# Kernel optimization log

Hardware: AMD Instinct MI355X
Metric: run time of the kernel (lower is better)

Reference implementation:

```python
import jax, jax.numpy as jnp
import numpy as np

N, D, E, H, K = 4096, 512, 32, 128, 4  # tokens, d_model, n_experts, expert hidden, top-k


def setup_inputs() -> dict:
    key = jax.random.key(0)
    k0, k1, k2, k3 = jax.random.split(key, 4)
    x = jax.random.normal(k0, (N, D), dtype=jnp.float32)
    # router weights, init std = d**-0.5 (matches get_initializer std)
    expert_sel = jax.random.normal(k1, (E, D), dtype=jnp.float32) * (D ** -0.5)
    # per-expert MLP weights (Linear stores [out, in]; we keep [E, in, out] layout)
    w1 = jax.random.normal(k2, (E, D, H), dtype=jnp.float32) * (D ** -0.5)
    w2 = jax.random.normal(k3, (E, H, D), dtype=jnp.float32) * (H ** -0.5)
    return {"x": x, "expert_sel": expert_sel, "w1": w1, "w2": w2}


def reference(x, expert_sel, w1, w2):
    # routing: sigmoid selection, top-k experts per token
    scores = jax.nn.sigmoid(x @ expert_sel.T)          # [N, E]
    gate_vals, gate_idx = jax.lax.top_k(scores, K)     # [N, K]
    # dense gate matrix with only top-k nonzero (sparse dispatch/combine weights)
    gate = (jax.nn.one_hot(gate_idx, E, dtype=x.dtype) * gate_vals[..., None]).sum(-2)  # [N, E]
    # per-expert MLP; gating at hidden is exact since experts have no bias:
    # gate * (relu(x W1) W2) == (gate * relu(x W1)) W2
    h = jax.nn.relu(jnp.einsum('nd,edh->neh', x, w1)) * gate[..., None]  # [N, E, H]
    y = jnp.einsum('neh,ehv->nv', h, w2)               # [N, D]
    return y
```

## Files before the change

kernel.cpp:

```cpp
#include <hip/hip_runtime.h>
#include <hip/hip_bf16.h>

#define NTOK 4096
#define DM   512
#define NE   32
#define HD   128
#define TK   4
#define RB   512
#define SLOTW 32

typedef unsigned short u16;
typedef unsigned int   u32;
typedef u16   u16x4 __attribute__((ext_vector_type(4)));
typedef u16   u16x8 __attribute__((ext_vector_type(8)));
typedef short short8 __attribute__((ext_vector_type(8)));
typedef float f32x4 __attribute__((ext_vector_type(4)));
typedef int   int2v __attribute__((ext_vector_type(2)));

__device__ __forceinline__ u16 f2bf(float f) {
    union { float f; u32 u; } v; v.f = f;
    return (u16)((v.u + 0x7FFFu + ((v.u >> 16) & 1u)) >> 16);
}
__device__ __forceinline__ float bf2f(u16 h) {
    union { u32 u; float f; } v; v.u = ((u32)h) << 16; return v.f;
}

__global__ __launch_bounds__(256) void prep_kernel(const float* __restrict__ x,
                                                   const float* __restrict__ sel,
                                                   const float* __restrict__ w1,
                                                   const float* __restrict__ w2,
                                                   int* __restrict__ blk_cnt,
                                                   u32* __restrict__ done,
                                                   int* __restrict__ tok_list,
                                                   float* __restrict__ gate_list,
                                                   u16* __restrict__ xbf,
                                                   u16* __restrict__ wf1,
                                                   u16* __restrict__ wf2) {
    __shared__ __align__(16) float  xs[8][520];
    __shared__ double sc[8][33];
    __shared__ int    pk_e[32];
    __shared__ float  pk_g[32];
    int tid = threadIdx.x;
    int wv = tid >> 6, lane = tid & 63;

    if (blockIdx.x >= RB) {
        int m = lane & 15, q = lane >> 4;
        int f0 = ((blockIdx.x - RB) * 4 + wv) * 2;
        const float* in[2]; u16* outp[2]; int Nd[2];
#pragma unroll
        for (int u = 0; u < 2; ++u) {
            int w = f0 + u;
            if (w < 4096) {
                int e = w >> 7, rem = w & 127, ks = rem >> 3, nt = rem & 7;
                in[u] = w1 + (size_t)e * DM * HD + (size_t)(32 * ks + q * 8) * HD + 16 * nt + m;
                Nd[u] = HD;
                outp[u] = wf1 + (size_t)w * 512 + lane * 8;
            } else {
                int wl = w - 4096, e = wl >> 7, rem = wl & 127, ks = rem >> 5, nt = rem & 31;
                in[u] = w2 + (size_t)e * HD * DM + (size_t)(32 * ks + q * 8) * DM + 16 * nt + m;
                Nd[u] = DM;
                outp[u] = wf2 + (size_t)wl * 512 + lane * 8;
            }
        }
        float v[2][8];
#pragma unroll
        for (int u = 0; u < 2; ++u)
#pragma unroll
            for (int j = 0; j < 8; ++j) v[u][j] = in[u][(size_t)j * Nd[u]];
#pragma unroll
        for (int u = 0; u < 2; ++u) {
            u16x8 h;
#pragma unroll
            for (int j = 0; j < 8; ++j) h[j] = f2bf(v[u][j]);
            *(u16x8*)outp[u] = h;
        }
        return;
    }

    int bl = blockIdx.x;
    int tb = bl * 8;
    if (tid < 8) done[tb + tid] = 0u;
#pragma unroll
    for (int rep = 0; rep < 4; ++rep) {
        int idx = (rep * 256 + tid) * 4;
        int row = idx >> 9, col = idx & 511;
        f32x4 v = *(const f32x4*)(x + (size_t)(tb + row) * DM + col);
        *(f32x4*)&xs[row][col] = v;
        u16x4 h;
#pragma unroll
        for (int j = 0; j < 4; ++j) h[j] = f2bf(v[j]);
        *(u16x4*)(xbf + (size_t)(tb + row) * DM + col) = h;
    }
    __syncthreads();

    {
        int tok = tid & 7, e = tid >> 3;
        const float* sp = sel + (size_t)e * DM;
        const float* xp = xs[tok];
        double pa = 0.0, pb = 0.0, pc = 0.0, pd = 0.0;
#pragma unroll 4
        for (int j = 0; j < 512; j += 16) {
            f32x4 x0 = *(const f32x4*)(xp + j);
            f32x4 x1 = *(const f32x4*)(xp + j + 4);
            f32x4 x2 = *(const f32x4*)(xp + j + 8);
            f32x4 x3 = *(const f32x4*)(xp + j + 12);
            f32x4 s0 = *(const f32x4*)(sp + j);
            f32x4 s1 = *(const f32x4*)(sp + j + 4);
            f32x4 s2 = *(const f32x4*)(sp + j + 8);
            f32x4 s3 = *(const f32x4*)(sp + j + 12);
#pragma unroll
            for (int k = 0; k < 4; ++k) {
                pa = fma((double)x0[k], (double)s0[k], pa);
                pb = fma((double)x1[k], (double)s1[k], pb);
                pc = fma((double)x2[k], (double)s2[k], pc);
                pd = fma((double)x3[k], (double)s3[k], pd);
            }
        }
        sc[tok][e] = (pa + pb) + (pc + pd);
    }
    __syncthreads();

    if (tid < 8) {
        unsigned mask = 0;
        for (int k = 0; k < TK; ++k) {
            double best = -1e300; int be = 0;
            for (int ee = 0; ee < NE; ++ee) {
                double v = sc[tid][ee];
                if (!((mask >> ee) & 1u) && v > best) { best = v; be = ee; }
            }
            mask |= 1u << be;
            pk_e[tid * 4 + k] = be;
            pk_g[tid * 4 + k] = 1.0f / (1.0f + __expf(-(float)best));
        }
    }
    __syncthreads();

    if (tid < NE) {
        int e2 = tid, cnt = 0;
        int base = (e2 * RB + bl) * SLOTW;
#pragma unroll
        for (int i = 0; i < 32; ++i) {
            if (pk_e[i] == e2) {
                tok_list[base + cnt]  = ((i & 3) << 16) | (tb + (i >> 2));
                gate_list[base + cnt] = pk_g[i];
                ++cnt;
            }
        }
        blk_cnt[e2 * RB + bl] = cnt;
    }
}

__global__ __launch_bounds__(256, 2) void moe_mlp_kernel(const u16* __restrict__ xbf,
                                                         const u16* __restrict__ wf1,
                                                         const u16* __restrict__ wf2,
                                                         const int* __restrict__ blk_cnt,
                                                         const int* __restrict__ tok_list,
                                                         const float* __restrict__ gate_list,
                                                         u32* __restrict__ done,
                                                         u16* __restrict__ part,
                                                         float* __restrict__ out,
                                                         int use_part) {
    __shared__ int   s_tot[4];
    __shared__ int   s_red[4][4];
    __shared__ int   s_pref[RB + 1];
    __shared__ int   s_ent[32];
    __shared__ float s_gate[32];
    __shared__ int   s_win[32];
    __shared__ __align__(16) u16 Hm[32][136];
    __shared__ __align__(16) u16 Ct[16][520];

    int tid = threadIdx.x;
    int wv = tid >> 6, lane = tid & 63;
    int xcd = blockIdx.x & 7, idx0 = blockIdx.x >> 3;

#pragma unroll
    for (int j = 0; j < 4; ++j) {
        int2v v = *(const int2v*)&blk_cnt[(size_t)(xcd + 8 * j) * RB + tid * 2];
        int s = v[0] + v[1];
#pragma unroll
        for (int off = 32; off >= 1; off >>= 1) s += __shfl_down(s, off);
        if (lane == 0) s_red[wv][j] = s;
    }
    __syncthreads();
    if (tid < 4) s_tot[tid] = s_red[0][tid] + s_red[1][tid] + s_red[2][tid] + s_red[3][tid];
    __syncthreads();

    int c0 = s_tot[0], c1 = s_tot[1], c2 = s_tot[2], c3 = s_tot[3];
    int n0 = (c0 + 31) >> 5, n1 = (c1 + 31) >> 5, n2 = (c2 + 31) >> 5, n3 = (c3 + 31) >> 5;
    int tot = n0 + n1 + n2 + n3;

    int m = lane & 15, q = lane >> 4;
    int r = wv >> 1, c = wv & 1;
    int e_last = -1;

    for (int idx = idx0; idx < tot; idx += 128) {
        int e2, t2, cc;
        if (idx < n0)                { e2 = xcd;      t2 = idx;                cc = c0; }
        else if (idx < n0 + n1)      { e2 = xcd + 8;  t2 = idx - n0;           cc = c1; }
        else if (idx < n0 + n1 + n2) { e2 = xcd + 16; t2 = idx - n0 - n1;      cc = c2; }
        else                         { e2 = xcd + 24; t2 = idx - n0 - n1 - n2; cc = c3; }
        int rows = cc - t2 * 32; if (rows > 32) rows = 32;

        __syncthreads();

        if (e2 != e_last) {
            int2v v = *(const int2v*)&blk_cnt[(size_t)e2 * RB + tid * 2];
            int lsum = v[0] + v[1];
            int incl = lsum;
#pragma unroll
            for (int off = 1; off < 64; off <<= 1) {
                int t3 = __shfl_up(incl, off);
                if (lane >= off) incl += t3;
            }
            if (lane == 63) s_red[0][wv] = incl;
            __syncthreads();
            int woff = 0;
#pragma unroll
            for (int w2 = 0; w2 < 4; ++w2) if (w2 < wv) woff += s_red[0][w2];
            int excl = woff + incl - lsum;
            s_pref[tid * 2 + 0] = excl;
            s_pref[tid * 2 + 1] = excl + v[0];
            if (tid == 255) s_pref[RB] = excl + lsum;
            e_last = e2;
            __syncthreads();
        }

        if (tid < 32) {
            int row = t2 * 32 + tid;
            bool val = tid < rows;
            int rr = val ? row : 0;
            int lo = 0, hi = RB;
            while (hi - lo > 1) { int mid = (lo + hi) >> 1; if (s_pref[mid] <= rr) lo = mid; else hi = mid; }
            int sub = rr - s_pref[lo];
            s_ent[tid]  = tok_list[((size_t)e2 * RB + lo) * SLOTW + sub];
            s_gate[tid] = val ? gate_list[((size_t)e2 * RB + lo) * SLOTW + sub] : 0.0f;
        }
        __syncthreads();

        const u16* w1f = wf1 + (size_t)e2 * (128 * 512);
        const u16* w2f = wf2 + (size_t)e2 * (128 * 512);
        const u16* a0 = xbf + (size_t)(s_ent[16 * r + m] & 0xFFFF) * DM + q * 8;

        short8 ab[2][2];
        short8 bb[2][2][4];
#pragma unroll
        for (int kk = 0; kk < 2; ++kk) {
            ab[0][kk] = *(const short8*)(a0 + 32 * kk);
            const u16* bp = w1f + (size_t)kk * 4096 + (size_t)(4 * c) * 512 + lane * 8;
#pragma unroll
            for (int n = 0; n < 4; ++n) bb[0][kk][n] = *(const short8*)(bp + n * 512);
        }
        f32x4 acc[4];
#pragma unroll
        for (int n = 0; n < 4; ++n) acc[n] = (f32x4){0.f, 0.f, 0.f, 0.f};

#pragma unroll
        for (int kp = 0; kp < 8; ++kp) {
            int cur = kp & 1, nxt = cur ^ 1;
            if (kp < 7) {
                int ks0 = 2 * (kp + 1);
#pragma unroll
                for (int kk = 0; kk < 2; ++kk) {
                    ab[nxt][kk] = *(const short8*)(a0 + 32 * (ks0 + kk));
                    const u16* bp = w1f + (size_t)(ks0 + kk) * 4096 + (size_t)(4 * c) * 512 + lane * 8;
#pragma unroll
                    for (int n = 0; n < 4; ++n) bb[nxt][kk][n] = *(const short8*)(bp + n * 512);
                }
            }
#pragma unroll
            for (int kk = 0; kk < 2; ++kk)
#pragma unroll
                for (int n = 0; n < 4; ++n)
                    acc[n] = __builtin_amdgcn_mfma_f32_16x16x32_bf16(ab[cur][kk],
                                                                     bb[cur][kk][n],
                                                                     acc[n], 0, 0, 0);
        }

        {
            int rb = 16 * r + q * 4;
#pragma unroll
            for (int n = 0; n < 4; ++n)
#pragma unroll
                for (int rr2 = 0; rr2 < 4; ++rr2)
                    Hm[rb + rr2][64 * c + 16 * n + m] =
                        f2bf(fmaxf(acc[n][rr2], 0.f) * s_gate[rb + rr2]);
        }

        short8 cb[2][8];
        {
            const u16* bp = w2f + (size_t)(wv * 8) * 512 + lane * 8;
#pragma unroll
            for (int n = 0; n < 8; ++n) cb[0][n] = *(const short8*)(bp + n * 512);
        }
        __syncthreads();

        f32x4 acc2[2][8];
#pragma unroll
        for (int i = 0; i < 2; ++i)
#pragma unroll
            for (int n = 0; n < 8; ++n) acc2[i][n] = (f32x4){0.f, 0.f, 0.f, 0.f};
#pragma unroll
        for (int ks = 0; ks < 4; ++ks) {
            int cur = ks & 1, nxt = cur ^ 1;
            if (ks < 3) {
                const u16* bp = w2f + (size_t)((ks + 1) * 32 + wv * 8) * 512 + lane * 8;
#pragma unroll
                for (int n = 0; n < 8; ++n) cb[nxt][n] = *(const short8*)(bp + n * 512);
            }
            short8 h0 = *(const short8*)&Hm[m][32 * ks + q * 8];
            short8 h1 = *(const short8*)&Hm[16 + m][32 * ks + q * 8];
#pragma unroll
            for (int n = 0; n < 8; ++n) {
                acc2[0][n] = __builtin_amdgcn_mfma_f32_16x16x32_bf16(h0, cb[cur][n], acc2[0][n], 0, 0, 0);
                acc2[1][n] = __builtin_amdgcn_mfma_f32_16x16x32_bf16(h1, cb[cur][n], acc2[1][n], 0, 0, 0);
            }
        }

#pragma unroll
        for (int i = 0; i < 2; ++i) {
            if (i) __syncthreads();
            {
                int rb = q * 4;
#pragma unroll
                for (int n = 0; n < 8; ++n)
#pragma unroll
                    for (int rr2 = 0; rr2 < 4; ++rr2)
                        Ct[rb + rr2][128 * wv + 16 * n + m] = f2bf(acc2[i][n][rr2]);
            }
            __syncthreads();
#pragma unroll
            for (int rep = 0; rep < 4; ++rep) {
                int rl = rep * 4 + wv;
                int rt = 16 * i + rl;
                u16x8 v = *(const u16x8*)&Ct[rl][lane * 8];
                if (rt < rows) {
                    int en = s_ent[rt];
                    int tk = en & 0xFFFF, sl2 = en >> 16;
                    if (use_part) {
                        *(u16x8*)(part + ((size_t)tk * TK + sl2) * DM + lane * 8) = v;
                    } else {
                        float* op = out + (size_t)tk * DM + lane * 8;
#pragma unroll
                        for (int j = 0; j < 8; ++j) atomicAdd(&op[j], bf2f(v[j]));
                    }
                }
            }
        }
        __syncthreads();

        if (use_part) {
            if (tid < 32) {
                int w = 0;
                if (tid < rows) {
                    int tk = s_ent[tid] & 0xFFFF;
                    u32 old = __hip_atomic_fetch_add(&done[tk], 1u, __ATOMIC_ACQ_REL,
                                                     __HIP_MEMORY_SCOPE_AGENT);
                    if (old == 3u) w = tk + 1;
                }
                s_win[tid] = w;
            }
            __syncthreads();
            for (int ws2 = wv; ws2 < 32; ws2 += 4) {
                int tw = s_win[ws2];
                if (!tw) continue;
                int t = tw - 1;
                const u16* pp = part + (size_t)t * (TK * DM) + lane * 8;
                float s[8] = {0, 0, 0, 0, 0, 0, 0, 0};
#pragma unroll
                for (int k = 0; k < TK; ++k) {
                    u16x8 p = *(const u16x8*)(pp + (size_t)k * DM);
#pragma unroll
                    for (int j = 0; j < 8; ++j) s[j] += bf2f(p[j]);
                }
                float* op = out + (size_t)t * DM + lane * 8;
                *(f32x4*)(op)     = (f32x4){s[0], s[1], s[2], s[3]};
                *(f32x4*)(op + 4) = (f32x4){s[4], s[5], s[6], s[7]};
            }
        }
    }
}

extern "C" void kernel_launch(void* const* d_in, const int* in_sizes, int n_in,
                              void* d_out, int out_size, void* d_ws, size_t ws_size,
                              hipStream_t stream) {
    (void)in_sizes; (void)n_in; (void)out_size;
    const float* x   = (const float*)d_in[0];
    const float* sel = (const float*)d_in[1];
    const float* w1  = (const float*)d_in[2];
    const float* w2  = (const float*)d_in[3];
    float* out = (float*)d_out;

    char* ws = (char*)d_ws;
    int*   blk_cnt   = (int*)(ws);
    u32*   done      = (u32*)(ws + (size_t)NE * RB * 4);
    int*   tok_list  = (int*)(ws + (size_t)NE * RB * 4 + NTOK * 4);
    float* gate_list = (float*)((char*)tok_list + (size_t)NE * RB * SLOTW * 4);
    u16*   xbf  = (u16*)((char*)gate_list + (size_t)NE * RB * SLOTW * 4);
    u16*   wf1  = xbf + (size_t)NTOK * DM;
    u16*   wf2  = wf1 + (size_t)NE * HD * DM;
    u16*   part = wf2 + (size_t)NE * HD * DM;

    size_t need = (size_t)NE * RB * 4 + NTOK * 4 + 2 * (size_t)NE * RB * SLOTW * 4
                + (size_t)NTOK * DM * 2 + 2 * (size_t)NE * HD * DM * 2
                + (size_t)NTOK * TK * DM * 2;
    int use_part = (ws_size >= need) ? 1 : 0;

    if (!use_part)
        hipMemsetAsync(d_out, 0, (size_t)NTOK * DM * sizeof(float), stream);

    prep_kernel<<<1536, 256, 0, stream>>>(x, sel, w1, w2, blk_cnt, done, tok_list,
                                          gate_list, xbf, wf1, wf2);
    moe_mlp_kernel<<<1024, 256, 0, stream>>>(xbf, wf1, wf2, blk_cnt, tok_list,
                                             gate_list, done, part, out, use_part);
}
```

Measured before the change: 141.4 us.

## Replace atomic last-arriver combine with separate combine kernel, raise occupancy

Removes the per-token done counters and the atomic fetch-add that let the last-arriving block sum the four bf16 partials, and moves that reduction into a standalone combine kernel launched after the MLP kernel. This drops the per-block barrier, the agent-scope atomics and the serialized tail work from the main kernel. The launch-bounds occupancy hint is also raised from 2 to 4 blocks per CU, which may force register spilling. The cost is an extra kernel launch and a full re-read of the partial buffer.

```diff
diff --git a/kernel.cpp b/kernel.cpp
--- a/kernel.cpp
+++ b/kernel.cpp
@@ -30,7 +30,6 @@
                                                    const float* __restrict__ w1,
                                                    const float* __restrict__ w2,
                                                    int* __restrict__ blk_cnt,
-                                                   u32* __restrict__ done,
                                                    int* __restrict__ tok_list,
                                                    float* __restrict__ gate_list,
                                                    u16* __restrict__ xbf,
@@ -79,7 +78,6 @@
 
     int bl = blockIdx.x;
     int tb = bl * 8;
-    if (tid < 8) done[tb + tid] = 0u;
 #pragma unroll
     for (int rep = 0; rep < 4; ++rep) {
         int idx = (rep * 256 + tid) * 4;
@@ -150,13 +148,12 @@
     }
 }
 
-__global__ __launch_bounds__(256, 2) void moe_mlp_kernel(const u16* __restrict__ xbf,
+__global__ __launch_bounds__(256, 4) void moe_mlp_kernel(const u16* __restrict__ xbf,
                                                          const u16* __restrict__ wf1,
                                                          const u16* __restrict__ wf2,
                                                          const int* __restrict__ blk_cnt,
                                                          const int* __restrict__ tok_list,
                                                          const float* __restrict__ gate_list,
-                                                         u32* __restrict__ done,
                                                          u16* __restrict__ part,
                                                          float* __restrict__ out,
                                                          int use_part) {
@@ -165,7 +162,6 @@
     __shared__ int   s_pref[RB + 1];
     __shared__ int   s_ent[32];
     __shared__ float s_gate[32];
-    __shared__ int   s_win[32];
     __shared__ __align__(16) u16 Hm[32][136];
     __shared__ __align__(16) u16 Ct[16][520];
 
@@ -346,38 +342,24 @@
                 }
             }
         }
-        __syncthreads();
-
-        if (use_part) {
-            if (tid < 32) {
-                int w = 0;
-                if (tid < rows) {
-                    int tk = s_ent[tid] & 0xFFFF;
-                    u32 old = __hip_atomic_fetch_add(&done[tk], 1u, __ATOMIC_ACQ_REL,
-                                                     __HIP_MEMORY_SCOPE_AGENT);
-                    if (old == 3u) w = tk + 1;
-                }
-                s_win[tid] = w;
-            }
-            __syncthreads();
-            for (int ws2 = wv; ws2 < 32; ws2 += 4) {
-                int tw = s_win[ws2];
-                if (!tw) continue;
-                int t = tw - 1;
-                const u16* pp = part + (size_t)t * (TK * DM) + lane * 8;
-                float s[8] = {0, 0, 0, 0, 0, 0, 0, 0};
-#pragma unroll
-                for (int k = 0; k < TK; ++k) {
-                    u16x8 p = *(const u16x8*)(pp + (size_t)k * DM);
-#pragma unroll
-                    for (int j = 0; j < 8; ++j) s[j] += bf2f(p[j]);
-                }
-                float* op = out + (size_t)t * DM + lane * 8;
-                *(f32x4*)(op)     = (f32x4){s[0], s[1], s[2], s[3]};
-                *(f32x4*)(op + 4) = (f32x4){s[4], s[5], s[6], s[7]};
-            }
-        }
-    }
+    }
+}
+
+__global__ __launch_bounds__(256) void combine_kernel(const u16* __restrict__ part,
+                                                      float* __restrict__ out) {
+    int g = blockIdx.x * 256 + threadIdx.x;
+    int t = g >> 6, c8 = (g & 63) << 3;
+    const u16* pp = part + (size_t)t * (TK * DM) + c8;
+    float s[8] = {0, 0, 0, 0, 0, 0, 0, 0};
+#pragma unroll
+    for (int k = 0; k < TK; ++k) {
+        u16x8 p = *(const u16x8*)(pp + (size_t)k * DM);
+#pragma unroll
+        for (int j = 0; j < 8; ++j) s[j] += bf2f(p[j]);
+    }
+    float* op = out + (size_t)t * DM + c8;
+    *(f32x4*)(op)     = (f32x4){s[0], s[1], s[2], s[3]};
+    *(f32x4*)(op + 4) = (f32x4){s[4], s[5], s[6], s[7]};
 }
 
 extern "C" void kernel_launch(void* const* d_in, const int* in_sizes, int n_in,
@@ -392,15 +374,14 @@
 
     char* ws = (char*)d_ws;
     int*   blk_cnt   = (int*)(ws);
-    u32*   done      = (u32*)(ws + (size_t)NE * RB * 4);
-    int*   tok_list  = (int*)(ws + (size_t)NE * RB * 4 + NTOK * 4);
+    int*   tok_list  = (int*)(ws + (size_t)NE * RB * 4);
     float* gate_list = (float*)((char*)tok_list + (size_t)NE * RB * SLOTW * 4);
     u16*   xbf  = (u16*)((char*)gate_list + (size_t)NE * RB * SLOTW * 4);
     u16*   wf1  = xbf + (size_t)NTOK * DM;
     u16*   wf2  = wf1 + (size_t)NE * HD * DM;
     u16*   part = wf2 + (size_t)NE * HD * DM;
 
-    size_t need = (size_t)NE * RB * 4 + NTOK * 4 + 2 * (size_t)NE * RB * SLOTW * 4
+    size_t need = (size_t)NE * RB * 4 + 2 * (size_t)NE * RB * SLOTW * 4
                 + (size_t)NTOK * DM * 2 + 2 * (size_t)NE * HD * DM * 2
                 + (size_t)NTOK * TK * DM * 2;
     int use_part = (ws_size >= need) ? 1 : 0;
@@ -408,8 +389,10 @@
     if (!use_part)
         hipMemsetAsync(d_out, 0, (size_t)NTOK * DM * sizeof(float), stream);
 
-    prep_kernel<<<1536, 256, 0, stream>>>(x, sel, w1, w2, blk_cnt, done, tok_list,
+    prep_kernel<<<1536, 256, 0, stream>>>(x, sel, w1, w2, blk_cnt, tok_list,
                                           gate_list, xbf, wf1, wf2);
     moe_mlp_kernel<<<1024, 256, 0, stream>>>(xbf, wf1, wf2, blk_cnt, tok_list,
-                                             gate_list, done, part, out, use_part);
-}
+                                             gate_list, part, out, use_part);
+    if (use_part)
+        combine_kernel<<<NTOK * DM / 8 / 256, 256, 0, stream>>>(part, out);
+}
```

Result: faster. 126.3 us (-10.7%).
